# Performance work log

Measured on AMD Instinct MI355X. Metric: run time of the kernel, lower is better.

The kernel has to match this reference:

```python
import jax, jax.numpy as jnp
import numpy as np

K = 4
TEMP = 34.0
KS = 3
PAD = 1
STRIDE = 1


def setup_inputs() -> dict:
    key = jax.random.key(0)
    k0, k1, k2, k3, k4, k5 = jax.random.split(key, 6)
    B, C, H, W = 32, 256, 56, 56
    OC = 256
    HID = int(C * 0.25) + 1  # 65
    x = jax.random.normal(k0, (B, C, H, W), jnp.float32)
    # kaiming-ish scales for the 1x1 attention convs (treated as matmuls)
    w_fc1 = jax.random.normal(k1, (HID, C), jnp.float32) * np.float32(np.sqrt(2.0 / C))
    w_fc2 = jax.random.normal(k2, (K, HID), jnp.float32) * np.float32(np.sqrt(2.0 / HID))
    b_fc2 = jnp.zeros((K,), jnp.float32)
    # positive step sizes for numerical sanity (torch inits randn then overwrites at init_state)
    alpha = jax.random.uniform(k3, (K, 1), jnp.float32, minval=0.05, maxval=1.0)
    weight = jax.random.normal(k4, (K, OC, C, KS, KS), jnp.float32) * 0.05
    bias_w = jax.random.normal(k5, (K, OC), jnp.float32) * 0.01
    return dict(x=x, w_fc1=w_fc1, w_fc2=w_fc2, b_fc2=b_fc2, alpha=alpha,
                weight=weight, bias_w=bias_w)


def _round_ste(v):
    # round_pass: forward round, backward identity
    return v + jax.lax.stop_gradient(jnp.round(v) - v)


def _lsq_quant(w2d, alpha):
    # Faithful to the torch LSQQuantizer forward (eval path): divide by per-row
    # alpha, clamp ONLY scalar elements [0,0],[1,0],[2,0] (as the torch code does),
    # then straight-through round and rescale. grad_scale copies into .data and
    # therefore has no effect on values or the autograd graph.
    d = w2d / alpha  # (K, M)
    d = d.at[0, 0].set(jnp.clip(d[0, 0], -2.0, 1.0))   # 2-bit range
    d = d.at[1, 0].set(jnp.clip(d[1, 0], -4.0, 3.0))   # 3-bit range
    d = d.at[2, 0].set(jnp.clip(d[2, 0], -8.0, 7.0))   # 4-bit range
    return _round_ste(d) * alpha


def reference(x, w_fc1, w_fc2, b_fc2, alpha, weight, bias_w):
    B, C, H, W = x.shape
    Kk, OC = bias_w.shape
    # attention2d: global avg pool -> 1x1 conv -> relu -> 1x1 conv (+bias)
    pooled = x.mean(axis=(2, 3))                     # (B, C)
    h = jax.nn.relu(pooled @ w_fc1.T)                # (B, HID)
    raw = h @ w_fc2.T + b_fc2                        # (B, K)
    # gradient_approximation: forward = one-hot(argmax), backward = softmax(x/T)
    soft = jax.nn.softmax(raw / TEMP, axis=1)
    hard = jax.nn.one_hot(jnp.argmax(raw, axis=1), Kk, dtype=raw.dtype)
    attn = soft + jax.lax.stop_gradient(hard - soft)  # (B, K)
    # LSQ-quantize flattened expert weights, then per-sample aggregation
    wq = _lsq_quant(weight.reshape(Kk, -1), alpha)   # (K, OC*C*KS*KS)
    agg_w = (attn @ wq).reshape(B, OC, C, KS, KS)    # per-sample kernels
    agg_b = attn @ bias_w                            # (B, OC)
    # per-sample conv2d (equivalent to the groups=batch trick)
    def conv1(xb, wb):
        return jax.lax.conv_general_dilated(
            xb[None], wb, (STRIDE, STRIDE), [(PAD, PAD), (PAD, PAD)],
            dimension_numbers=('NCHW', 'OIHW', 'NCHW'))[0]
    out = jax.vmap(conv1)(x, agg_w) + agg_b[:, :, None, None]  # (B, OC, H, W)
    return (out, raw)
```

## Files before the change

### kernel.cpp

```cpp
#include <hip/hip_runtime.h>
#include <hip/hip_bf16.h>

typedef __attribute__((ext_vector_type(8))) short short8;
typedef __attribute__((ext_vector_type(4))) float f32x4;

#define XPAD_OFF   0u
#define WQ_OFF     62717952u
#define POOL_OFF   67436544u
#define IDX_OFF    67469312u

__device__ __forceinline__ void gl_lds16(const void* g, void* l) {
  __builtin_amdgcn_global_load_lds(
      (const __attribute__((address_space(1))) unsigned int*)g,
      (__attribute__((address_space(3))) unsigned int*)l, 16, 0, 0);
}

__global__ __launch_bounds__(256) void pool_kernel(const float* __restrict__ x,
                                                   float* __restrict__ pooled) {
  __shared__ float sbuf[256];
  const int bc = blockIdx.x;
  const float* p = x + (size_t)bc * 3136;
  float s = 0.f;
  for (int i = threadIdx.x; i < 3136; i += 256) s += p[i];
  sbuf[threadIdx.x] = s;
  __syncthreads();
  for (int st = 128; st > 0; st >>= 1) {
    if (threadIdx.x < st) sbuf[threadIdx.x] += sbuf[threadIdx.x + st];
    __syncthreads();
  }
  if (threadIdx.x == 0) pooled[bc] = sbuf[0] * (1.0f / 3136.0f);
}

__global__ __launch_bounds__(128) void fc_argmax_kernel(
    const float* __restrict__ pooled, const float* __restrict__ w_fc1,
    const float* __restrict__ w_fc2, const float* __restrict__ b_fc2,
    float* __restrict__ raw_out, int* __restrict__ idx) {
  __shared__ float h[65];
  __shared__ float raws[4];
  const int b = blockIdx.x, t = threadIdx.x;
  if (t < 65) {
    float s = 0.f;
    const float* pb = pooled + b * 256;
    const float* wr = w_fc1 + t * 256;
    for (int c = 0; c < 256; ++c) s += pb[c] * wr[c];
    h[t] = s > 0.f ? s : 0.f;
  }
  __syncthreads();
  if (t < 4) {
    float s = b_fc2[t];
    const float* wr = w_fc2 + t * 65;
    for (int j = 0; j < 65; ++j) s += h[j] * wr[j];
    raws[t] = s;
    raw_out[b * 4 + t] = s;
  }
  __syncthreads();
  if (t == 0) {
    int best = 0; float bv = raws[0];
    for (int k = 1; k < 4; ++k) if (raws[k] > bv) { bv = raws[k]; best = k; }
    idx[b] = best;
  }
}

__global__ __launch_bounds__(256) void quant_kernel(
    const float* __restrict__ weight, const float* __restrict__ alpha,
    __hip_bfloat16* __restrict__ Wq) {
  const unsigned d = blockIdx.x * 256u + threadIdx.x;
  const unsigned cl   = d & 7u;
  const unsigned lane = (d >> 3) & 63u;
  const unsigned arow = lane & 15u;
  const unsigned kgrp = lane >> 4;
  const unsigned i    = (d >> 9) & 3u;
  const unsigned wm   = (d >> 11) & 1u;
  const unsigned cb32 = (d >> 12) & 7u;
  const unsigned rest = d >> 15;
  const unsigned tap  = rest % 9u;
  const unsigned q    = rest / 9u;
  const unsigned ot   = q & 1u;
  const unsigned k    = q >> 1;
  const unsigned oc = ot * 128u + wm * 64u + i * 16u + arow;
  const unsigned ch = cb32 * 32u + kgrp * 8u + cl;
  const float a = alpha[k];
  float v = weight[(size_t)k * 589824u + oc * 2304u + ch * 9u + tap] / a;
  if (oc == 0u && ch == 0u && tap == 0u) {
    if (k == 0u)      v = fminf(fmaxf(v, -2.f), 1.f);
    else if (k == 1u) v = fminf(fmaxf(v, -4.f), 3.f);
    else if (k == 2u) v = fminf(fmaxf(v, -8.f), 7.f);
  }
  Wq[d] = __float2bfloat16(rintf(v) * a);
}

__global__ __launch_bounds__(256) void padx_kernel(const float* __restrict__ x,
                                                   __hip_bfloat16* __restrict__ Xpad) {
  __shared__ float T[56 * 132];
  const int yp = blockIdx.x;
  const int c0 = blockIdx.y * 128;
  const int b  = blockIdx.z;
  const int tid = threadIdx.x;
  __hip_bfloat16* orow = Xpad + ((size_t)(b * 58 + yp) * 66) * 256 + c0;
  const short8 zero8 = (short8){0, 0, 0, 0, 0, 0, 0, 0};
  const bool rowin = (yp >= 1 && yp <= 56);
  if (rowin) {
    const float* xbase = x + (((size_t)b * 256 + c0) * 56 + (yp - 1)) * 56;
    for (int i = tid; i < 128 * 56; i += 256) {
      const int cl = i / 56, px = i - cl * 56;
      T[px * 132 + cl] = xbase[cl * 3136 + px];
    }
    __syncthreads();
    for (int i = tid; i < 896; i += 256) {
      const int px = i >> 4, cg = (i & 15) * 8;
      union { short8 v; __hip_bfloat16 e[8]; } u;
      #pragma unroll
      for (int r = 0; r < 8; ++r) u.e[r] = __float2bfloat16(T[px * 132 + cg + r]);
      *(short8*)&orow[(px + 1) * 256 + cg] = u.v;
    }
    for (int i = tid; i < 160; i += 256) {
      const int pi = i >> 4, cg = (i & 15) * 8;
      const int xp = (pi == 0) ? 0 : 56 + pi;
      *(short8*)&orow[xp * 256 + cg] = zero8;
    }
  } else {
    for (int i = tid; i < 66 * 16; i += 256) {
      const int xp = i >> 4, cg = (i & 15) * 8;
      *(short8*)&orow[xp * 256 + cg] = zero8;
    }
  }
}

__global__ __launch_bounds__(256, 2) void conv_kernel(
    const __hip_bfloat16* __restrict__ Xpad, const __hip_bfloat16* __restrict__ Wq,
    const int* __restrict__ idx, const float* __restrict__ bias_w,
    float* __restrict__ out) {
  __shared__ __attribute__((aligned(16))) __hip_bfloat16 Xs[19456];

  const int tid = threadIdx.x;
  const int lane = tid & 63;
  const int w = tid >> 6;
  const int wm = w & 1;
  const int wn = w >> 1;

  const int pt = blockIdx.x;
  const int ot = blockIdx.y;
  const int b = blockIdx.z;
  const int Y0 = pt * 2;
  const int OC0 = ot * 128;
  const int kb = idx[b];

  const __hip_bfloat16* xb = Xpad + (size_t)b * (58 * 66 * 256);
  const short8* W0 = (const short8*)Wq + (size_t)(kb * 2 + ot) * 36864;

  f32x4 acc[4][4];
  #pragma unroll
  for (int i = 0; i < 4; ++i)
    #pragma unroll
    for (int j = 0; j < 4; ++j) acc[i][j] = (f32x4){0.f, 0.f, 0.f, 0.f};

  const int arow = lane & 15;
  const int kgrp = lane >> 4;

  for (int cc = 0; cc < 4; ++cc) {
    __syncthreads();
    for (int s = w; s < 38; s += 4) {
      int ch = s * 64 + lane;
      if (ch > 2375) ch = 2375;
      int p = ch / 9, cpart = ch - p * 9;
      if (cpart > 7) cpart = 7;
      const int r = p / 66, xc = p - r * 66;
      gl_lds16(xb + (((Y0 + r) * 66 + xc) * 256 + cc * 64 + cpart * 8),
               (char*)Xs + s * 1024);
    }
    __syncthreads();

    short8 af[4], afn[4];
    #pragma unroll
    for (int i = 0; i < 4; ++i)
      af[i] = W0[((0 * 8 + cc * 2 + 0) * 2 + wm) * 4 * 64 + i * 64 + lane];

    #pragma unroll
    for (int t = 0; t < 18; ++t) {
      const int tap = t >> 1, h = t & 1;
      const int dy = tap / 3, dx = tap - dy * 3;
      short8 bfr[4];
      const int xsrow = (wn + dy) * 66;
      #pragma unroll
      for (int j = 0; j < 4; ++j) {
        const int col = j * 16 + arow + dx;
        bfr[j] = *(const short8*)&Xs[(xsrow + col) * 72 + h * 32 + kgrp * 8];
      }
      if (t < 17) {
        const int tn = t + 1, tapn = tn >> 1, hn = tn & 1;
        #pragma unroll
        for (int i = 0; i < 4; ++i)
          afn[i] = W0[((tapn * 8 + cc * 2 + hn) * 2 + wm) * 4 * 64 + i * 64 + lane];
      }
      #pragma unroll
      for (int i = 0; i < 4; ++i)
        #pragma unroll
        for (int j = 0; j < 4; ++j)
          acc[i][j] = __builtin_amdgcn_mfma_f32_16x16x32_bf16(
              af[i], bfr[j], acc[i][j], 0, 0, 0);
      #pragma unroll
      for (int i = 0; i < 4; ++i) af[i] = afn[i];
    }
  }

  const float* biasb = bias_w + kb * 256 + OC0;
  #pragma unroll
  for (int i = 0; i < 4; ++i) {
    const int ocbase = wm * 64 + i * 16 + (lane >> 4) * 4;
    #pragma unroll
    for (int j = 0; j < 4; ++j) {
      const int pl = wn * 64 + j * 16 + (lane & 15);
      const int xcol = pl & 63;
      if (xcol < 56) {
        const int y = Y0 + (pl >> 6);
        #pragma unroll
        for (int r = 0; r < 4; ++r) {
          const int oc = ocbase + r;
          out[(((size_t)b * 256 + OC0 + oc) * 56 + y) * 56 + xcol] =
              acc[i][j][r] + biasb[oc];
        }
      }
    }
  }
}

extern "C" void kernel_launch(void* const* d_in, const int* in_sizes, int n_in,
                              void* d_out, int out_size, void* d_ws, size_t ws_size,
                              hipStream_t stream) {
  const float* x      = (const float*)d_in[0];
  const float* w_fc1  = (const float*)d_in[1];
  const float* w_fc2  = (const float*)d_in[2];
  const float* b_fc2  = (const float*)d_in[3];
  const float* alpha  = (const float*)d_in[4];
  const float* weight = (const float*)d_in[5];
  const float* bias_w = (const float*)d_in[6];

  float* out = (float*)d_out;
  float* raw_out = out + (size_t)32 * 256 * 56 * 56;

  char* ws = (char*)d_ws;
  __hip_bfloat16* Xpad = (__hip_bfloat16*)(ws + XPAD_OFF);
  __hip_bfloat16* Wq   = (__hip_bfloat16*)(ws + WQ_OFF);
  float* pooled        = (float*)(ws + POOL_OFF);
  int* idx             = (int*)(ws + IDX_OFF);

  pool_kernel<<<8192, 256, 0, stream>>>(x, pooled);
  fc_argmax_kernel<<<32, 128, 0, stream>>>(pooled, w_fc1, w_fc2, b_fc2, raw_out, idx);
  quant_kernel<<<9216, 256, 0, stream>>>(weight, alpha, Wq);
  padx_kernel<<<dim3(58, 2, 32), 256, 0, stream>>>(x, Xpad);
  conv_kernel<<<dim3(28, 2, 32), 256, 0, stream>>>(Xpad, Wq, idx, bias_w, out);
}
```

Measured before the change: 397.9 us.

## Fuse pooling into padding pass and double-buffer conv LDS staging with swizzle

Removes the separate pooling kernel by accumulating per-channel row sums inside the padding transpose with atomics, so x is read once fewer. The conv kernel now stages 32-channel slices into two LDS buffers with an XOR swizzle, prefetching the next slice while computing the current one. It also raises the occupancy hint to 4 blocks per CU. Atomic float summation changes the order of the pooled accumulation, which could flip an argmax in near-tie cases.

```diff
diff --git a/kernel.cpp b/kernel.cpp
--- a/kernel.cpp
+++ b/kernel.cpp
@@ -13,22 +13,6 @@
   __builtin_amdgcn_global_load_lds(
       (const __attribute__((address_space(1))) unsigned int*)g,
       (__attribute__((address_space(3))) unsigned int*)l, 16, 0, 0);
-}
-
-__global__ __launch_bounds__(256) void pool_kernel(const float* __restrict__ x,
-                                                   float* __restrict__ pooled) {
-  __shared__ float sbuf[256];
-  const int bc = blockIdx.x;
-  const float* p = x + (size_t)bc * 3136;
-  float s = 0.f;
-  for (int i = threadIdx.x; i < 3136; i += 256) s += p[i];
-  sbuf[threadIdx.x] = s;
-  __syncthreads();
-  for (int st = 128; st > 0; st >>= 1) {
-    if (threadIdx.x < st) sbuf[threadIdx.x] += sbuf[threadIdx.x + st];
-    __syncthreads();
-  }
-  if (threadIdx.x == 0) pooled[bc] = sbuf[0] * (1.0f / 3136.0f);
 }
 
 __global__ __launch_bounds__(128) void fc_argmax_kernel(
@@ -43,6 +27,7 @@
     const float* pb = pooled + b * 256;
     const float* wr = w_fc1 + t * 256;
     for (int c = 0; c < 256; ++c) s += pb[c] * wr[c];
+    s *= (1.0f / 3136.0f);
     h[t] = s > 0.f ? s : 0.f;
   }
   __syncthreads();
@@ -90,7 +75,8 @@
 }
 
 __global__ __launch_bounds__(256) void padx_kernel(const float* __restrict__ x,
-                                                   __hip_bfloat16* __restrict__ Xpad) {
+                                                   __hip_bfloat16* __restrict__ Xpad,
+                                                   float* __restrict__ pooled) {
   __shared__ float T[56 * 132];
   const int yp = blockIdx.x;
   const int c0 = blockIdx.y * 128;
@@ -106,6 +92,11 @@
       T[px * 132 + cl] = xbase[cl * 3136 + px];
     }
     __syncthreads();
+    if (tid < 128) {
+      float s = 0.f;
+      for (int px = 0; px < 56; ++px) s += T[px * 132 + tid];
+      atomicAdd(pooled + b * 256 + c0 + tid, s);
+    }
     for (int i = tid; i < 896; i += 256) {
       const int px = i >> 4, cg = (i & 15) * 8;
       union { short8 v; __hip_bfloat16 e[8]; } u;
@@ -126,11 +117,11 @@
   }
 }
 
-__global__ __launch_bounds__(256, 2) void conv_kernel(
+__global__ __launch_bounds__(256, 4) void conv_kernel(
     const __hip_bfloat16* __restrict__ Xpad, const __hip_bfloat16* __restrict__ Wq,
     const int* __restrict__ idx, const float* __restrict__ bias_w,
     float* __restrict__ out) {
-  __shared__ __attribute__((aligned(16))) __hip_bfloat16 Xs[19456];
+  __shared__ __attribute__((aligned(16))) __hip_bfloat16 Xs[17408];
 
   const int tid = threadIdx.x;
   const int lane = tid & 63;
@@ -157,40 +148,49 @@
   const int arow = lane & 15;
   const int kgrp = lane >> 4;
 
-  for (int cc = 0; cc < 4; ++cc) {
-    __syncthreads();
-    for (int s = w; s < 38; s += 4) {
-      int ch = s * 64 + lane;
-      if (ch > 2375) ch = 2375;
-      int p = ch / 9, cpart = ch - p * 9;
-      if (cpart > 7) cpart = 7;
+  auto stage = [&](int cbh, int bufsel) {
+    char* dst = (char*)Xs + bufsel * 17408;
+    for (int k = w; k < 17; k += 4) {
+      const int s = k * 64 + lane;
+      int p = s >> 2;
+      if (p > 263) p = 263;
+      const int g = (s & 3) ^ ((p >> 1) & 3);
       const int r = p / 66, xc = p - r * 66;
-      gl_lds16(xb + (((Y0 + r) * 66 + xc) * 256 + cc * 64 + cpart * 8),
-               (char*)Xs + s * 1024);
-    }
-    __syncthreads();
-
-    short8 af[4], afn[4];
+      gl_lds16(xb + (((Y0 + r) * 66 + xc) * 256 + cbh * 32 + g * 8),
+               dst + k * 1024);
+    }
+  };
+
+  stage(0, 0);
+  __syncthreads();
+
+  short8 af[4], afn[4];
+  #pragma unroll
+  for (int i = 0; i < 4; ++i)
+    af[i] = W0[(size_t)(wm * 256) + i * 64 + lane];
+
+  for (int cbh = 0; cbh < 8; ++cbh) {
+    const __hip_bfloat16* cur = Xs + (cbh & 1) * 8704;
+    if (cbh < 7) stage(cbh + 1, (cbh + 1) & 1);
+
     #pragma unroll
-    for (int i = 0; i < 4; ++i)
-      af[i] = W0[((0 * 8 + cc * 2 + 0) * 2 + wm) * 4 * 64 + i * 64 + lane];
-
-    #pragma unroll
-    for (int t = 0; t < 18; ++t) {
-      const int tap = t >> 1, h = t & 1;
+    for (int tap = 0; tap < 9; ++tap) {
       const int dy = tap / 3, dx = tap - dy * 3;
       short8 bfr[4];
-      const int xsrow = (wn + dy) * 66;
       #pragma unroll
       for (int j = 0; j < 4; ++j) {
-        const int col = j * 16 + arow + dx;
-        bfr[j] = *(const short8*)&Xs[(xsrow + col) * 72 + h * 32 + kgrp * 8];
+        const int p = (wn + dy) * 66 + j * 16 + arow + dx;
+        const int slot = p * 4 + (kgrp ^ ((p >> 1) & 3));
+        bfr[j] = *(const short8*)&cur[slot * 8];
       }
-      if (t < 17) {
-        const int tn = t + 1, tapn = tn >> 1, hn = tn & 1;
+      if (tap < 8) {
         #pragma unroll
         for (int i = 0; i < 4; ++i)
-          afn[i] = W0[((tapn * 8 + cc * 2 + hn) * 2 + wm) * 4 * 64 + i * 64 + lane];
+          afn[i] = W0[(((tap + 1) * 8 + cbh) * 2 + wm) * 256 + i * 64 + lane];
+      } else if (cbh < 7) {
+        #pragma unroll
+        for (int i = 0; i < 4; ++i)
+          afn[i] = W0[((cbh + 1) * 2 + wm) * 256 + i * 64 + lane];
       }
       #pragma unroll
       for (int i = 0; i < 4; ++i)
@@ -201,6 +201,7 @@
       #pragma unroll
       for (int i = 0; i < 4; ++i) af[i] = afn[i];
     }
+    __syncthreads();
   }
 
   const float* biasb = bias_w + kb * 256 + OC0;
@@ -244,9 +245,9 @@
   float* pooled        = (float*)(ws + POOL_OFF);
   int* idx             = (int*)(ws + IDX_OFF);
 
-  pool_kernel<<<8192, 256, 0, stream>>>(x, pooled);
+  hipMemsetAsync(pooled, 0, 32 * 256 * sizeof(float), stream);
+  padx_kernel<<<dim3(58, 2, 32), 256, 0, stream>>>(x, Xpad, pooled);
+  quant_kernel<<<9216, 256, 0, stream>>>(weight, alpha, Wq);
   fc_argmax_kernel<<<32, 128, 0, stream>>>(pooled, w_fc1, w_fc2, b_fc2, raw_out, idx);
-  quant_kernel<<<9216, 256, 0, stream>>>(weight, alpha, Wq);
-  padx_kernel<<<dim3(58, 2, 32), 256, 0, stream>>>(x, Xpad);
   conv_kernel<<<dim3(28, 2, 32), 256, 0, stream>>>(Xpad, Wq, idx, bias_w, out);
 }
```

After: 372.5 us. 6.4% less time.
